# Optimization experiments

Hardware: AMD Instinct MI355X
Metric: run time of the kernel (lower is better)

Reference implementation:

```python
import jax, jax.numpy as jnp
import numpy as np

P = 7  # output_size


def _axis_weights(start, length, dim):
    """Per-roi 1D interpolation matrix A [R, P, dim] such that the roi_align
    output separates as out = Ay @ fm @ Ax^T (torchvision roi_align,
    aligned=False, sampling_ratio=-1 i.e. adaptive ceil(bin) samples)."""
    S = int(np.ceil(dim / P))  # max samples per bin (rois lie inside the image)
    bin_sz = length / P                               # [R]
    grid = jnp.ceil(length / P).astype(jnp.int32)     # adaptive samples per bin, [R]
    g = grid.astype(jnp.float32)[:, None, None]       # [R,1,1]
    s = jnp.arange(S, dtype=jnp.float32)              # [S]
    ph = jnp.arange(P, dtype=jnp.float32)             # [P]
    # sample coordinate: start + ph*bin + (s+0.5)*bin/grid  -> [R,P,S]
    coord = (start[:, None, None] + ph[None, :, None] * bin_sz[:, None, None]
             + (s[None, None, :] + 0.5) * bin_sz[:, None, None] / g)
    valid = (coord >= -1.0) & (coord <= dim)
    c = jnp.maximum(coord, 0.0)
    low = jnp.floor(c).astype(jnp.int32)
    hi_clamp = low >= dim - 1
    low = jnp.where(hi_clamp, dim - 1, low)
    high = jnp.where(hi_clamp, dim - 1, low + 1)
    cv = jnp.where(hi_clamp, low.astype(jnp.float32), c)
    l = cv - low.astype(jnp.float32)
    smask = (s[None, None, :] < g) & valid            # mask unused samples
    w = smask.astype(jnp.float32) / g                 # 1/count split per axis
    w_low = (1.0 - l) * w
    w_high = l * w
    R = start.shape[0]
    r_idx = jnp.arange(R)[:, None, None]
    p_idx = jnp.arange(P)[None, :, None]
    A = jnp.zeros((R, P, dim), dtype=jnp.float32)
    A = A.at[r_idx, p_idx, low].add(w_low)
    A = A.at[r_idx, p_idx, high].add(w_high)
    return A


def _roi_align(fm, rois):
    # fm: [C,H,W]; rois: [R,4] = (x1,y1,x2,y2); spatial_scale=1.0
    C, H, W = fm.shape
    x1, y1, x2, y2 = rois[:, 0], rois[:, 1], rois[:, 2], rois[:, 3]
    roi_w = jnp.maximum(x2 - x1, 1.0)
    roi_h = jnp.maximum(y2 - y1, 1.0)
    Ay = _axis_weights(y1, roi_h, H)                  # [R,P,H]
    Ax = _axis_weights(x1, roi_w, W)                  # [R,P,W]
    tmp = jnp.einsum('rph,chw->rcpw', Ay, fm)         # [R,C,P,W]
    return jnp.einsum('rcpw,rqw->rcpq', tmp, Ax)      # [R,C,P,P]


def _per_image(fm, b, g):
    # fm: [C,H,W], b: [N,4] boxes, g: [M,4] gt boxes
    N, M = b.shape[0], g.shape[0]
    # context boxes: union (min of mins, max of maxes) of every (box, gt) pair
    x1 = jnp.minimum(b[:, None, 0], g[None, :, 0])
    y1 = jnp.minimum(b[:, None, 1], g[None, :, 1])
    x2 = jnp.maximum(b[:, None, 2], g[None, :, 2])
    y2 = jnp.maximum(b[:, None, 3], g[None, :, 3])
    ctx = jnp.stack([x1, y1, x2, y2], axis=-1).reshape(N * M, 4)
    feats = _roi_align(fm, jnp.concatenate([b, ctx], axis=0))  # [N+N*M,C,P,P]
    box_f = feats[:N]
    ctx_mean = feats[N:].reshape(N, M, feats.shape[1], P, P).mean(axis=1)
    return box_f + ctx_mean                            # [N,C,P,P]


def setup_inputs() -> dict:
    key = jax.random.key(0)
    B, C, H, W, N, M = 2, 256, 56, 56, 64, 8
    k1, k2, k3, k4, k5 = jax.random.split(key, 5)
    feature_map = jax.random.normal(k1, (B, C, H, W), dtype=jnp.float32)
    # boxes inside the feature map, max side 0.35*H so adaptive grid <= ceil(H/7)
    b_xy1 = jax.random.uniform(k2, (B, N, 2), minval=0.0, maxval=0.64 * H)
    b_wh = jax.random.uniform(k3, (B, N, 2), minval=4.0, maxval=0.35 * H)
    boxes = jnp.concatenate([b_xy1, b_xy1 + b_wh], axis=-1).astype(jnp.float32)
    g_xy1 = jax.random.uniform(k4, (B, M, 2), minval=0.0, maxval=0.64 * H)
    g_wh = jax.random.uniform(k5, (B, M, 2), minval=4.0, maxval=0.35 * H)
    gt_boxes = jnp.concatenate([g_xy1, g_xy1 + g_wh], axis=-1).astype(jnp.float32)
    return {"feature_map": feature_map, "boxes": boxes, "gt_boxes": gt_boxes}


def reference(feature_map, boxes, gt_boxes):
    # returns [B, N, C, P, P] (stacked version of the per-image list output)
    return jax.vmap(_per_image)(feature_map, boxes, gt_boxes)
```

## Files before the change

kernel.cpp:

```cpp
#include <hip/hip_runtime.h>

#define B_ 2
#define C_ 256
#define H_ 56
#define W_ 56
#define N_ 64
#define M_ 8
#define P_ 7
#define Y2_ (H_/2)
#define Y4_ (H_/4)
#define SCTX_ 4
#define JPN_ (1 + (M_)*SCTX_)
#define WROW_ 8

typedef _Float16 half2v __attribute__((ext_vector_type(2)));

#if __has_builtin(__builtin_amdgcn_fdot2)
#define FDOT2(a, b, c) __builtin_amdgcn_fdot2((a), (b), (c), false)
#else
static __device__ __forceinline__ float FDOT2(half2v a, half2v b, float c) {
    return fmaf((float)a.x, (float)b.x, fmaf((float)a.y, (float)b.y, c));
}
#endif

#define F_FMT4 0
#define N_FMT4 (B_*Y4_*W_*C_*2)
#define F_OUTS (F_FMT4 + N_FMT4)
#define N_OUTS (B_*N_*49*C_)
#define WS_ELEMS (F_OUTS + N_OUTS)

#define PREP_T (B_*Y4_*4*2)
#define PREP_N (PREP_T + 784)

__global__ __launch_bounds__(256) void k_prep(const float* __restrict__ fm,
                                              float* __restrict__ ws_f) {
    __shared__ float t[28 * 257 + 8];
    int bid = blockIdx.x;
    int tid = (int)threadIdx.x;

    if (bid < PREP_T) {
        int xh = bid & 1;
        int cg = (bid >> 1) & 3;
        int y4 = (bid >> 3) % Y4_;
        int b  = (bid >> 3) / Y4_;
        int c0 = cg * 64, x0 = xh * 28;
        for (int e = tid; e < 64 * 4 * 28; e += 256) {
            int c_l = e / 112, rem = e % 112;
            int y_l = rem / 28, x_l = rem % 28;
            t[x_l * 257 + y_l * 64 + c_l] =
                fm[(((size_t)b * C_ + c0 + c_l) * H_ + 4 * y4 + y_l) * W_ + x0 + x_l];
        }
        __syncthreads();
        uint2* dst = (uint2*)ws_f;
        for (int e = tid; e < 28 * 64; e += 256) {
            int x_l = e >> 6, c_l = e & 63;
            const float* p = &t[x_l * 257 + c_l];
            half2v lo, hi; uint2 o;
            lo.x = (_Float16)p[0];   lo.y = (_Float16)p[64];
            hi.x = (_Float16)p[128]; hi.y = (_Float16)p[192];
            o.x = __builtin_bit_cast(unsigned int, lo);
            o.y = __builtin_bit_cast(unsigned int, hi);
            dst[(((size_t)b * Y4_ + y4) * W_ + x0 + x_l) * (size_t)C_ + c0 + c_l] = o;
        }
        return;
    }

    {
        int tz = (bid - PREP_T) * 256 + tid;
        float4 z = {0.0f, 0.0f, 0.0f, 0.0f};
        float4* dst = (float4*)(ws_f + F_OUTS);
        dst[tz * 2]     = z;
        dst[tz * 2 + 1] = z;
    }
}

__global__ __launch_bounds__(256, 4) void k_main(const float* __restrict__ ws_f,
                                                 const float* __restrict__ boxes,
                                                 const float* __restrict__ gt,
                                                 float* __restrict__ outs) {
    __shared__ float        s_wyf[H_][WROW_];
    __shared__ unsigned int s_wy2[Y2_ * WROW_];
    __shared__ float        s_ax[W_][WROW_];

    int bid = blockIdx.x;
    int j   = bid % JPN_;
    int n   = (bid / JPN_) & (N_ - 1);
    int b   = bid / (JPN_ * N_);
    int k, s;
    if (j == 0) { k = 0; s = 0; }
    else        { k = 1 + ((j - 1) >> 2); s = (j - 1) & 3; }
    int p0, p1;
    if (k == 0) { p0 = 0; p1 = P_ - 1; }
    else        { p0 = 2 * s; p1 = (2 * s + 1 < P_) ? 2 * s + 1 : P_ - 1; }
    int tid  = (int)threadIdx.x;
    int c    = tid;

    const float* bp = boxes + ((size_t)b * N_ + n) * 4;
    float bx1, by1, bx2, by2;
    if (k == 0) {
        bx1 = bp[0]; by1 = bp[1]; bx2 = bp[2]; by2 = bp[3];
    } else {
        const float* gp = gt + ((size_t)b * M_ + (k - 1)) * 4;
        bx1 = fminf(bp[0], gp[0]); by1 = fminf(bp[1], gp[1]);
        bx2 = fmaxf(bp[2], gp[2]); by2 = fmaxf(bp[3], gp[3]);
    }
    float rw = fmaxf(bx2 - bx1, 1.0f);
    float rh = fmaxf(by2 - by1, 1.0f);

    for (int e = tid; e < H_ * WROW_; e += 256) ((float*)s_wyf)[e] = 0.0f;
    for (int e = tid; e < W_ * WROW_; e += 256) ((float*)s_ax)[e] = 0.0f;
    __syncthreads();

    if (tid < P_) {
        int p = tid;
        float bin = rh / 7.0f;
        float gf  = ceilf(bin);
        int   g   = (int)gf;
        float ivg = 1.0f / gf;
        float start = by1 + (float)p * bin;
        for (int ss = 0; ss < g; ++ss) {
            float coord = start + ((float)ss + 0.5f) * bin * ivg;
            if (coord < -1.0f || coord > (float)H_) continue;
            float cc = fmaxf(coord, 0.0f);
            int low = (int)floorf(cc);
            int high; float l;
            if (low >= H_ - 1) { low = H_ - 1; high = H_ - 1; l = 0.0f; }
            else               { high = low + 1; l = cc - (float)low; }
            s_wyf[low][p]  += (1.0f - l) * ivg;
            s_wyf[high][p] += l * ivg;
        }
    } else if (tid >= 64 && tid < 64 + P_) {
        int p = tid - 64;
        float bin = rw / 7.0f;
        float gf  = ceilf(bin);
        int   g   = (int)gf;
        float ivg = 1.0f / gf;
        float fs  = (k == 0) ? ivg : ivg * (1.0f / (float)M_);
        float start = bx1 + (float)p * bin;
        for (int ss = 0; ss < g; ++ss) {
            float coord = start + ((float)ss + 0.5f) * bin * ivg;
            if (coord < -1.0f || coord > (float)W_) continue;
            float cc = fmaxf(coord, 0.0f);
            int low = (int)floorf(cc);
            int high; float l;
            if (low >= W_ - 1) { low = W_ - 1; high = W_ - 1; l = 0.0f; }
            else               { high = low + 1; l = cc - (float)low; }
            s_ax[low][p]  += (1.0f - l) * fs;
            s_ax[high][p] += l * fs;
        }
    }
    __syncthreads();

    if (tid < Y2_ * WROW_) {
        int q2 = tid >> 3, col = tid & 7;
        half2v h;
        if (col < P_) { h.x = (_Float16)s_wyf[2 * q2][col]; h.y = (_Float16)s_wyf[2 * q2 + 1][col]; }
        else          { h.x = (_Float16)0.0f; h.y = (_Float16)0.0f; }
        s_wy2[tid] = __builtin_bit_cast(unsigned int, h);
    } else if (k != 0) {
        int r = tid - 224;
#pragma unroll
        for (int px = 0; px < P_; ++px) {
            if (px < p0 || px > p1) {
                s_ax[r][px] = 0.0f;
                if (r + 32 < W_) s_ax[r + 32][px] = 0.0f;
            }
        }
    }
    __syncthreads();

    int xs, xe;
    if (k == 0) {
        xs = min(max((int)floorf(fmaxf(bx1, 0.0f)), 0), W_ - 1);
        xe = min(max((int)floorf(bx1 + rw) + 1, 0), W_ - 1) + 1;
    } else {
        float binw = rw * (1.0f / 7.0f);
        float lo_f = bx1 + (float)p0 * binw;
        float hi_f = bx1 + (float)(p1 + 1) * binw;
        xs = min(max((int)floorf(fmaxf(lo_f, 0.0f)), 0), W_ - 1);
        xe = min(max((int)floorf(fminf(hi_f, (float)W_)) + 1, 0), W_ - 1) + 1;
    }
    if (xs >= xe) return;

    int ylo = min(max((int)floorf(fmaxf(by1, 0.0f)), 0), H_ - 1);
    int yhi = min(max((int)floorf(by1 + rh) + 1, 0), H_ - 1) + 1;
    int ylo4 = ylo >> 2;
    int yhi4 = (yhi + 3) >> 2;

    const uint2* f4 = (const uint2*)ws_f + (size_t)b * (Y4_ * W_ * C_);

    float acc[49];
#pragma unroll
    for (int q = 0; q < 49; ++q) acc[q] = 0.0f;
    int live = 0;

    for (int x = xs; x < xe; x += 4) {
        float cs[4][P_];
#pragma unroll
        for (int i = 0; i < 4; ++i)
#pragma unroll
            for (int py = 0; py < P_; ++py) cs[i][py] = 0.0f;

        const uint2* cp = f4 + ((size_t)(ylo4 * W_ + x)) * C_ + c;
        for (int y4 = ylo4; y4 < yhi4; ++y4) {
            uint2 d0 = cp[0];
            uint2 d1 = cp[C_];
            uint2 d2 = cp[2 * C_];
            uint2 d3 = cp[3 * C_];
            uint4 wa0 = *(const uint4*)&s_wy2[(2 * y4) * WROW_];
            uint4 wb0 = *(const uint4*)&s_wy2[(2 * y4) * WROW_ + 4];
            uint4 wa1 = *(const uint4*)&s_wy2[(2 * y4 + 1) * WROW_];
            uint4 wb1 = *(const uint4*)&s_wy2[(2 * y4 + 1) * WROW_ + 4];
            half2v w0[7], w1[7];
            w0[0] = __builtin_bit_cast(half2v, wa0.x);
            w0[1] = __builtin_bit_cast(half2v, wa0.y);
            w0[2] = __builtin_bit_cast(half2v, wa0.z);
            w0[3] = __builtin_bit_cast(half2v, wa0.w);
            w0[4] = __builtin_bit_cast(half2v, wb0.x);
            w0[5] = __builtin_bit_cast(half2v, wb0.y);
            w0[6] = __builtin_bit_cast(half2v, wb0.z);
            w1[0] = __builtin_bit_cast(half2v, wa1.x);
            w1[1] = __builtin_bit_cast(half2v, wa1.y);
            w1[2] = __builtin_bit_cast(half2v, wa1.z);
            w1[3] = __builtin_bit_cast(half2v, wa1.w);
            w1[4] = __builtin_bit_cast(half2v, wb1.x);
            w1[5] = __builtin_bit_cast(half2v, wb1.y);
            w1[6] = __builtin_bit_cast(half2v, wb1.z);
            half2v v0a = __builtin_bit_cast(half2v, d0.x);
            half2v v0b = __builtin_bit_cast(half2v, d0.y);
            half2v v1a = __builtin_bit_cast(half2v, d1.x);
            half2v v1b = __builtin_bit_cast(half2v, d1.y);
            half2v v2a = __builtin_bit_cast(half2v, d2.x);
            half2v v2b = __builtin_bit_cast(half2v, d2.y);
            half2v v3a = __builtin_bit_cast(half2v, d3.x);
            half2v v3b = __builtin_bit_cast(half2v, d3.y);
#pragma unroll
            for (int py = 0; py < P_; ++py) {
                cs[0][py] = FDOT2(w1[py], v0b, FDOT2(w0[py], v0a, cs[0][py]));
                cs[1][py] = FDOT2(w1[py], v1b, FDOT2(w0[py], v1a, cs[1][py]));
                cs[2][py] = FDOT2(w1[py], v2b, FDOT2(w0[py], v2a, cs[2][py]));
                cs[3][py] = FDOT2(w1[py], v3b, FDOT2(w0[py], v3a, cs[3][py]));
            }
            cp += W_ * C_;
        }

#pragma unroll
        for (int i = 0; i < 4; ++i) {
            if (x + i < xe) {
                float av[8];
                *(float4*)(&av[0]) = *(const float4*)&s_ax[x + i][0];
                *(float4*)(&av[4]) = *(const float4*)&s_ax[x + i][4];
#pragma unroll
                for (int px = 0; px < P_; ++px) {
                    float w = av[px];
                    if (w != 0.0f) {
                        live |= 1 << px;
#pragma unroll
                        for (int py = 0; py < P_; ++py)
                            acc[py * P_ + px] = fmaf(w, cs[i][py], acc[py * P_ + px]);
                    }
                }
            }
        }
    }

    float* os = outs + ((size_t)b * N_ + n) * (49 * C_) + c;
#pragma unroll
    for (int px = 0; px < P_; ++px) {
        if (live & (1 << px)) {
#pragma unroll
            for (int py = 0; py < P_; ++py)
                atomicAdd(os + (py * P_ + px) * C_, acc[py * P_ + px]);
        }
    }
}

__global__ __launch_bounds__(256) void k_final(const float* __restrict__ outs,
                                               float* __restrict__ out) {
    __shared__ float t[49 * 65];
    int bid = blockIdx.x;
    int cg  = bid & 3;
    int bn  = bid >> 2;
    int tid = (int)threadIdx.x;
    const float* src = outs + (size_t)bn * (49 * C_) + cg * 64;
    for (int e = tid; e < 49 * 64; e += 256) {
        int q = e >> 6, c = e & 63;
        t[q * 65 + c] = src[q * C_ + c];
    }
    __syncthreads();
    float* dst = out + (size_t)bn * (C_ * 49) + (size_t)cg * 64 * 49;
    for (int e = tid; e < 64 * 49; e += 256) {
        int c = e / 49, q = e - c * 49;
        dst[e] = t[q * 65 + c];
    }
}

extern "C" void kernel_launch(void* const* d_in, const int* in_sizes, int n_in,
                              void* d_out, int out_size, void* d_ws, size_t ws_size,
                              hipStream_t stream) {
    const float* fm    = (const float*)d_in[0];
    const float* boxes = (const float*)d_in[1];
    const float* gt    = (const float*)d_in[2];
    float* ws_f = (float*)d_ws;
    float* out  = (float*)d_out;
    float* outs = ws_f + F_OUTS;

    k_prep<<<PREP_N, 256, 0, stream>>>(fm, ws_f);
    k_main<<<B_ * N_ * JPN_, 256, 0, stream>>>(ws_f, boxes, gt, outs);
    k_final<<<B_ * N_ * 4, 256, 0, stream>>>(outs, out);
}
```

Baseline: 149.7 us.

## Drop per-context x-strip split and use hipMemset for output zeroing

Each context ROI block now handles the full 7-column output instead of splitting it into four x-strips, so the main grid shrinks from 33 to 9 blocks per box. This removes the per-strip column masking and range logic, but each block now does more serial work and there is less parallelism overall. Zeroing of the accumulation buffer moves out of the prep kernel into a hipMemsetAsync call.

```diff
diff --git a/kernel.cpp b/kernel.cpp
--- a/kernel.cpp
+++ b/kernel.cpp
@@ -9,8 +9,7 @@
 #define P_ 7
 #define Y2_ (H_/2)
 #define Y4_ (H_/4)
-#define SCTX_ 4
-#define JPN_ (1 + (M_)*SCTX_)
+#define JR_ (1 + M_)
 #define WROW_ 8
 
 typedef _Float16 half2v __attribute__((ext_vector_type(2)));
@@ -30,7 +29,6 @@
 #define WS_ELEMS (F_OUTS + N_OUTS)
 
 #define PREP_T (B_*Y4_*4*2)
-#define PREP_N (PREP_T + 784)
 
 __global__ __launch_bounds__(256) void k_prep(const float* __restrict__ fm,
                                               float* __restrict__ ws_f) {
@@ -38,39 +36,28 @@
     int bid = blockIdx.x;
     int tid = (int)threadIdx.x;
 
-    if (bid < PREP_T) {
-        int xh = bid & 1;
-        int cg = (bid >> 1) & 3;
-        int y4 = (bid >> 3) % Y4_;
-        int b  = (bid >> 3) / Y4_;
-        int c0 = cg * 64, x0 = xh * 28;
-        for (int e = tid; e < 64 * 4 * 28; e += 256) {
-            int c_l = e / 112, rem = e % 112;
-            int y_l = rem / 28, x_l = rem % 28;
-            t[x_l * 257 + y_l * 64 + c_l] =
-                fm[(((size_t)b * C_ + c0 + c_l) * H_ + 4 * y4 + y_l) * W_ + x0 + x_l];
-        }
-        __syncthreads();
-        uint2* dst = (uint2*)ws_f;
-        for (int e = tid; e < 28 * 64; e += 256) {
-            int x_l = e >> 6, c_l = e & 63;
-            const float* p = &t[x_l * 257 + c_l];
-            half2v lo, hi; uint2 o;
-            lo.x = (_Float16)p[0];   lo.y = (_Float16)p[64];
-            hi.x = (_Float16)p[128]; hi.y = (_Float16)p[192];
-            o.x = __builtin_bit_cast(unsigned int, lo);
-            o.y = __builtin_bit_cast(unsigned int, hi);
-            dst[(((size_t)b * Y4_ + y4) * W_ + x0 + x_l) * (size_t)C_ + c0 + c_l] = o;
-        }
-        return;
-    }
-
-    {
-        int tz = (bid - PREP_T) * 256 + tid;
-        float4 z = {0.0f, 0.0f, 0.0f, 0.0f};
-        float4* dst = (float4*)(ws_f + F_OUTS);
-        dst[tz * 2]     = z;
-        dst[tz * 2 + 1] = z;
+    int xh = bid & 1;
+    int cg = (bid >> 1) & 3;
+    int y4 = (bid >> 3) % Y4_;
+    int b  = (bid >> 3) / Y4_;
+    int c0 = cg * 64, x0 = xh * 28;
+    for (int e = tid; e < 64 * 4 * 28; e += 256) {
+        int c_l = e / 112, rem = e % 112;
+        int y_l = rem / 28, x_l = rem % 28;
+        t[x_l * 257 + y_l * 64 + c_l] =
+            fm[(((size_t)b * C_ + c0 + c_l) * H_ + 4 * y4 + y_l) * W_ + x0 + x_l];
+    }
+    __syncthreads();
+    uint2* dst = (uint2*)ws_f;
+    for (int e = tid; e < 28 * 64; e += 256) {
+        int x_l = e >> 6, c_l = e & 63;
+        const float* p = &t[x_l * 257 + c_l];
+        half2v lo, hi; uint2 o;
+        lo.x = (_Float16)p[0];   lo.y = (_Float16)p[64];
+        hi.x = (_Float16)p[128]; hi.y = (_Float16)p[192];
+        o.x = __builtin_bit_cast(unsigned int, lo);
+        o.y = __builtin_bit_cast(unsigned int, hi);
+        dst[(((size_t)b * Y4_ + y4) * W_ + x0 + x_l) * (size_t)C_ + c0 + c_l] = o;
     }
 }
 
@@ -83,15 +70,9 @@
     __shared__ float        s_ax[W_][WROW_];
 
     int bid = blockIdx.x;
-    int j   = bid % JPN_;
-    int n   = (bid / JPN_) & (N_ - 1);
-    int b   = bid / (JPN_ * N_);
-    int k, s;
-    if (j == 0) { k = 0; s = 0; }
-    else        { k = 1 + ((j - 1) >> 2); s = (j - 1) & 3; }
-    int p0, p1;
-    if (k == 0) { p0 = 0; p1 = P_ - 1; }
-    else        { p0 = 2 * s; p1 = (2 * s + 1 < P_) ? 2 * s + 1 : P_ - 1; }
+    int k   = bid % JR_;
+    int n   = (bid / JR_) & (N_ - 1);
+    int b   = bid / (JR_ * N_);
     int tid  = (int)threadIdx.x;
     int c    = tid;
 
@@ -157,31 +138,11 @@
         if (col < P_) { h.x = (_Float16)s_wyf[2 * q2][col]; h.y = (_Float16)s_wyf[2 * q2 + 1][col]; }
         else          { h.x = (_Float16)0.0f; h.y = (_Float16)0.0f; }
         s_wy2[tid] = __builtin_bit_cast(unsigned int, h);
-    } else if (k != 0) {
-        int r = tid - 224;
-#pragma unroll
-        for (int px = 0; px < P_; ++px) {
-            if (px < p0 || px > p1) {
-                s_ax[r][px] = 0.0f;
-                if (r + 32 < W_) s_ax[r + 32][px] = 0.0f;
-            }
-        }
-    }
-    __syncthreads();
-
-    int xs, xe;
-    if (k == 0) {
-        xs = min(max((int)floorf(fmaxf(bx1, 0.0f)), 0), W_ - 1);
-        xe = min(max((int)floorf(bx1 + rw) + 1, 0), W_ - 1) + 1;
-    } else {
-        float binw = rw * (1.0f / 7.0f);
-        float lo_f = bx1 + (float)p0 * binw;
-        float hi_f = bx1 + (float)(p1 + 1) * binw;
-        xs = min(max((int)floorf(fmaxf(lo_f, 0.0f)), 0), W_ - 1);
-        xe = min(max((int)floorf(fminf(hi_f, (float)W_)) + 1, 0), W_ - 1) + 1;
-    }
-    if (xs >= xe) return;
-
+    }
+    __syncthreads();
+
+    int xs = min(max((int)floorf(fmaxf(bx1, 0.0f)), 0), W_ - 1);
+    int xe = min(max((int)floorf(bx1 + rw) + 1, 0), W_ - 1) + 1;
     int ylo = min(max((int)floorf(fmaxf(by1, 0.0f)), 0), H_ - 1);
     int yhi = min(max((int)floorf(by1 + rh) + 1, 0), H_ - 1) + 1;
     int ylo4 = ylo >> 2;
@@ -305,7 +266,8 @@
     float* out  = (float*)d_out;
     float* outs = ws_f + F_OUTS;
 
-    k_prep<<<PREP_N, 256, 0, stream>>>(fm, ws_f);
-    k_main<<<B_ * N_ * JPN_, 256, 0, stream>>>(ws_f, boxes, gt, outs);
+    hipMemsetAsync(outs, 0, (size_t)N_OUTS * sizeof(float), stream);
+    k_prep<<<PREP_T, 256, 0, stream>>>(fm, ws_f);
+    k_main<<<B_ * N_ * JR_, 256, 0, stream>>>(ws_f, boxes, gt, outs);
     k_final<<<B_ * N_ * 4, 256, 0, stream>>>(outs, out);
 }
```

Result: slower. 157.7 us (+5.4%).

## Split context ROI work by x-column range and software-prefetch next y row

Applied to the files above, without the earlier changes.

Context blocks now divide the ROI's x-column span evenly into four chunks instead of assigning two output bins per block and zeroing the other bins' x weights. Each block therefore accumulates all seven output columns over its slice of x, which is meant to balance load across the four split blocks and remove the weight-masking step. The inner y loop also loads the next row's feature data before computing the current row, to hide global-memory latency. This relies on the later reduction summing partial results across the split blocks; the prefetch adds registers and one redundant load on the last iteration.

```diff
diff --git a/kernel.cpp b/kernel.cpp
--- a/kernel.cpp
+++ b/kernel.cpp
@@ -89,9 +89,6 @@
     int k, s;
     if (j == 0) { k = 0; s = 0; }
     else        { k = 1 + ((j - 1) >> 2); s = (j - 1) & 3; }
-    int p0, p1;
-    if (k == 0) { p0 = 0; p1 = P_ - 1; }
-    else        { p0 = 2 * s; p1 = (2 * s + 1 < P_) ? 2 * s + 1 : P_ - 1; }
     int tid  = (int)threadIdx.x;
     int c    = tid;
 
@@ -157,33 +154,22 @@
         if (col < P_) { h.x = (_Float16)s_wyf[2 * q2][col]; h.y = (_Float16)s_wyf[2 * q2 + 1][col]; }
         else          { h.x = (_Float16)0.0f; h.y = (_Float16)0.0f; }
         s_wy2[tid] = __builtin_bit_cast(unsigned int, h);
-    } else if (k != 0) {
-        int r = tid - 224;
-#pragma unroll
-        for (int px = 0; px < P_; ++px) {
-            if (px < p0 || px > p1) {
-                s_ax[r][px] = 0.0f;
-                if (r + 32 < W_) s_ax[r + 32][px] = 0.0f;
-            }
-        }
     }
     __syncthreads();
 
-    int xs, xe;
-    if (k == 0) {
-        xs = min(max((int)floorf(fmaxf(bx1, 0.0f)), 0), W_ - 1);
-        xe = min(max((int)floorf(bx1 + rw) + 1, 0), W_ - 1) + 1;
-    } else {
-        float binw = rw * (1.0f / 7.0f);
-        float lo_f = bx1 + (float)p0 * binw;
-        float hi_f = bx1 + (float)(p1 + 1) * binw;
-        xs = min(max((int)floorf(fmaxf(lo_f, 0.0f)), 0), W_ - 1);
-        xe = min(max((int)floorf(fminf(hi_f, (float)W_)) + 1, 0), W_ - 1) + 1;
-    }
-    if (xs >= xe) return;
-
+    int xlo = min(max((int)floorf(fmaxf(bx1, 0.0f)), 0), W_ - 1);
+    int xhi = min(max((int)floorf(bx1 + rw) + 1, 0), W_ - 1) + 1;
     int ylo = min(max((int)floorf(fmaxf(by1, 0.0f)), 0), H_ - 1);
     int yhi = min(max((int)floorf(by1 + rh) + 1, 0), H_ - 1) + 1;
+    int xs, xe;
+    if (k == 0) { xs = xlo; xe = xhi; }
+    else {
+        int cw = (xhi - xlo + SCTX_ - 1) >> 2;
+        xs = xlo + s * cw;
+        xe = min(xs + cw, xhi);
+    }
+    if (xs >= xe) return;
+
     int ylo4 = ylo >> 2;
     int yhi4 = (yhi + 3) >> 2;
 
@@ -202,11 +188,19 @@
             for (int py = 0; py < P_; ++py) cs[i][py] = 0.0f;
 
         const uint2* cp = f4 + ((size_t)(ylo4 * W_ + x)) * C_ + c;
+
+        uint2 d0 = cp[0];
+        uint2 d1 = cp[C_];
+        uint2 d2 = cp[2 * C_];
+        uint2 d3 = cp[3 * C_];
         for (int y4 = ylo4; y4 < yhi4; ++y4) {
-            uint2 d0 = cp[0];
-            uint2 d1 = cp[C_];
-            uint2 d2 = cp[2 * C_];
-            uint2 d3 = cp[3 * C_];
+            size_t nstep = (y4 + 1 < yhi4) ? (size_t)(W_ * C_) : 0;
+            const uint2* cq = cp + nstep;
+            uint2 e0 = cq[0];
+            uint2 e1 = cq[C_];
+            uint2 e2 = cq[2 * C_];
+            uint2 e3 = cq[3 * C_];
+
             uint4 wa0 = *(const uint4*)&s_wy2[(2 * y4) * WROW_];
             uint4 wb0 = *(const uint4*)&s_wy2[(2 * y4) * WROW_ + 4];
             uint4 wa1 = *(const uint4*)&s_wy2[(2 * y4 + 1) * WROW_];
@@ -241,7 +235,8 @@
                 cs[2][py] = FDOT2(w1[py], v2b, FDOT2(w0[py], v2a, cs[2][py]));
                 cs[3][py] = FDOT2(w1[py], v3b, FDOT2(w0[py], v3a, cs[3][py]));
             }
-            cp += W_ * C_;
+            d0 = e0; d1 = e1; d2 = e2; d3 = e3;
+            cp = cq;
         }
 
 #pragma unroll
```

Result: no change. 149.4 us (-0.2%).
